# Performance work log

Measured on AMD Instinct MI355X. Metric: run time of the kernel, lower is better.

Reference implementation:

```python
import jax, jax.numpy as jnp
import numpy as np

D_MODEL = 512
D_QK = 512
H = 8
HEAD_DIM = D_QK // H   # 64
V_DIM = D_MODEL // H   # 64
PROJ_OUT = D_MODEL + 2 * D_QK + H  # 1544


def setup_inputs() -> dict:
    key = jax.random.key(0)
    k1, k2, k3, k4, k5 = jax.random.split(key, 5)
    B, S = 2, 2048
    x = jax.random.normal(k1, (B, S, D_MODEL), dtype=jnp.float32)
    s_in = 1.0 / np.sqrt(D_MODEL)
    Wvqkn_w = jax.random.uniform(k2, (PROJ_OUT, D_MODEL), jnp.float32, -s_in, s_in)
    Wvqkn_b = jax.random.uniform(k3, (PROJ_OUT,), jnp.float32, -s_in, s_in)
    out_w = jax.random.uniform(k4, (D_MODEL, D_MODEL), jnp.float32, -s_in, s_in)
    out_b = jax.random.uniform(k5, (D_MODEL,), jnp.float32, -s_in, s_in)
    return {"x": x, "Wvqkn_w": Wvqkn_w, "Wvqkn_b": Wvqkn_b,
            "out_w": out_w, "out_b": out_b}


def reference(x, Wvqkn_w, Wvqkn_b, out_w, out_b):
    B, S, _ = x.shape
    # fused qkvn projection
    vqkn = jnp.einsum('bsd,od->bso', x, Wvqkn_w) + Wvqkn_b  # [B,S,1544]
    v = vqkn[..., :D_MODEL]                                  # [B,S,512]
    qk = vqkn[..., D_MODEL:D_MODEL + 2 * D_QK]               # [B,S,1024]
    n = vqkn[..., D_MODEL + 2 * D_QK:]                       # [B,S,H]
    qk = qk.reshape(B, S, 2, H, HEAD_DIM)
    v = v.reshape(B, S, H, V_DIM)
    q, k = qk[:, :, 0], qk[:, :, 1]                          # approx_fn = identity
    # linear attention via cumulative KV state (scale=1.0, scale_B=False)
    kv = jnp.einsum('bshd,bsht->bshdt', k, v)                # [B,S,H,D,Dv]
    kv = jnp.cumsum(kv, axis=1)
    out = jnp.einsum('bshd,bshdt->bsht', q, kv)              # [B,S,H,Dv]
    # normalization gating: norm_fn = exp, no offset
    gate = jnp.exp(-jnp.exp(n))                              # [B,S,H]
    ctx = gate[..., None] * out
    ctx = ctx.reshape(B, S, D_MODEL)
    return jnp.einsum('bsd,od->bso', ctx, out_w) + out_b
```

## Files before the change

### kernel.cpp

```cpp
#include <hip/hip_runtime.h>
#include <hip/hip_bf16.h>
#include <math.h>

#define B_    2
#define S_    2048
#define DM    512
#define H_    8
#define PROJ  1544
#define NPAD1 1664
#define CHK   64
#define NC    32
#define BS_   4096
#define BH    16

typedef __attribute__((ext_vector_type(8))) short shortx8;
typedef __attribute__((ext_vector_type(4))) short shortx4;
typedef __attribute__((ext_vector_type(4))) float floatx4;

#define GCAST(p) ((const __attribute__((address_space(1))) void*)(p))
#define LCAST(p) ((__attribute__((address_space(3))) void*)(p))

__device__ inline short f2bf(float f) {
    __hip_bfloat16 h = __float2bfloat16(f);
    return *(short*)&h;
}
__device__ inline float bf2f(short s) {
    __hip_bfloat16 h = *(__hip_bfloat16*)&s;
    return __bfloat162float(h);
}
__device__ inline shortx8 read8(const short* buf, int row, int k) {
    return *(const shortx8*)&buf[row * 64 + ((((k >> 3) ^ (row & 7))) << 3)];
}

#define E1 ((size_t)BS_ * DM)
#define E2 ((size_t)NPAD1 * DM)
#define E3 ((size_t)DM * DM)
__global__ __launch_bounds__(256) void convert_all(const float* __restrict__ x,
                                                   const float* __restrict__ w1,
                                                   const float* __restrict__ w2,
                                                   short* __restrict__ xb,
                                                   short* __restrict__ w1b,
                                                   short* __restrict__ w2b) {
    size_t e = ((size_t)blockIdx.x * 256 + threadIdx.x) * 8;
    const float* src;
    short* dst;
    bool zero = false;
    if (e < E1) { src = x + e; dst = xb + e; }
    else if (e < E1 + E2) {
        size_t o = e - E1;
        dst = w1b + o;
        size_t row = o >> 9;
        if (row < PROJ) src = w1 + o; else { src = w1; zero = true; }
    } else if (e < E1 + E2 + E3) {
        size_t o = e - E1 - E2;
        src = w2 + o; dst = w2b + o;
    } else return;
    short out[8];
    if (zero) {
#pragma unroll
        for (int i = 0; i < 8; i++) out[i] = 0;
    } else {
        float4 f0 = *(const float4*)src;
        float4 f1 = *(const float4*)(src + 4);
        out[0] = f2bf(f0.x); out[1] = f2bf(f0.y); out[2] = f2bf(f0.z); out[3] = f2bf(f0.w);
        out[4] = f2bf(f1.x); out[5] = f2bf(f1.y); out[6] = f2bf(f1.z); out[7] = f2bf(f1.w);
    }
    *(shortx8*)dst = *(shortx8*)out;
}

__global__ __launch_bounds__(256) void gemm_mfma64(const short* __restrict__ A,
                                                   const short* __restrict__ Bw,
                                                   const float* __restrict__ bias,
                                                   float* __restrict__ C,
                                                   int N, int K) {
    __shared__ __align__(16) short As[64 * 64];
    __shared__ __align__(16) short Bs[128 * 64];
    const int tid  = threadIdx.x;
    const int wave = tid >> 6, lane = tid & 63;
    const int m0 = blockIdx.y * 64;
    const int n0 = blockIdx.x * 128;
    const int lrow = lane >> 3;
    const int swz  = ((lane & 7) ^ lrow) << 3;
    const int lm = lane & 15, q = lane >> 4;
    const int wc = wave * 32;
    floatx4 acc[4][2] = {};

    const short* gA0 = A  + (size_t)(m0 +      wave * 8 + lrow) * K + swz;
    const short* gA1 = A  + (size_t)(m0 + 32 + wave * 8 + lrow) * K + swz;
    const short* gB[4];
#pragma unroll
    for (int h = 0; h < 4; h++)
        gB[h] = Bw + (size_t)(n0 + h * 32 + wave * 8 + lrow) * K + swz;

    for (int k0 = 0; k0 < K; k0 += 64) {
        __builtin_amdgcn_global_load_lds(GCAST(gA0 + k0), LCAST(&As[(wave * 8) * 64]),        16, 0, 0);
        __builtin_amdgcn_global_load_lds(GCAST(gA1 + k0), LCAST(&As[(32 + wave * 8) * 64]),   16, 0, 0);
#pragma unroll
        for (int h = 0; h < 4; h++)
            __builtin_amdgcn_global_load_lds(GCAST(gB[h] + k0), LCAST(&Bs[(h * 32 + wave * 8) * 64]), 16, 0, 0);
        __syncthreads();
        shortx8 af[2][4], bw[2][2];
#pragma unroll
        for (int ks = 0; ks < 2; ks++) {
#pragma unroll
            for (int i = 0; i < 4; i++) af[ks][i] = read8(As, i * 16 + lm, ks * 32 + q * 8);
#pragma unroll
            for (int j = 0; j < 2; j++) bw[ks][j] = read8(Bs, wc + j * 16 + lm, ks * 32 + q * 8);
        }
#pragma unroll
        for (int ks = 0; ks < 2; ks++)
#pragma unroll
            for (int i = 0; i < 4; i++)
#pragma unroll
                for (int j = 0; j < 2; j++)
                    acc[i][j] = __builtin_amdgcn_mfma_f32_16x16x32_bf16(af[ks][i], bw[ks][j], acc[i][j], 0, 0, 0);
        __syncthreads();
    }
#pragma unroll
    for (int i = 0; i < 4; i++) {
        int rb = m0 + i * 16 + q * 4;
#pragma unroll
        for (int j = 0; j < 2; j++) {
            int col = n0 + wc + j * 16 + lm;
            float bv = bias[col];
#pragma unroll
            for (int r = 0; r < 4; r++)
                C[(size_t)(rb + r) * N + col] = acc[i][j][r] + bv;
        }
    }
}

__global__ __launch_bounds__(256) void gemm1_fused(const short* __restrict__ A,
                                                   const short* __restrict__ Bw,
                                                   const float* __restrict__ bias,
                                                   short* __restrict__ qb,
                                                   short* __restrict__ kb,
                                                   short* __restrict__ kTb,
                                                   short* __restrict__ vTb,
                                                   float* __restrict__ gateb) {
    __shared__ __align__(16) short As[64 * 64];
    __shared__ __align__(16) short Bs[128 * 64];
    const int K = DM;
    const int tid  = threadIdx.x;
    const int wave = tid >> 6, lane = tid & 63;
    const int m0 = blockIdx.y * 64;
    const int n0 = blockIdx.x * 128;
    const int lrow = lane >> 3;
    const int swz  = ((lane & 7) ^ lrow) << 3;
    const int lm = lane & 15, q = lane >> 4;
    const int wc = wave * 32;
    floatx4 acc[4][2] = {};

    const short* gA0 = A  + (size_t)(m0 +      wave * 8 + lrow) * K + swz;
    const short* gA1 = A  + (size_t)(m0 + 32 + wave * 8 + lrow) * K + swz;
    const short* gB[4];
#pragma unroll
    for (int h = 0; h < 4; h++)
        gB[h] = Bw + (size_t)(n0 + h * 32 + wave * 8 + lrow) * K + swz;

    for (int k0 = 0; k0 < K; k0 += 64) {
        __builtin_amdgcn_global_load_lds(GCAST(gA0 + k0), LCAST(&As[(wave * 8) * 64]),        16, 0, 0);
        __builtin_amdgcn_global_load_lds(GCAST(gA1 + k0), LCAST(&As[(32 + wave * 8) * 64]),   16, 0, 0);
#pragma unroll
        for (int h = 0; h < 4; h++)
            __builtin_amdgcn_global_load_lds(GCAST(gB[h] + k0), LCAST(&Bs[(h * 32 + wave * 8) * 64]), 16, 0, 0);
        __syncthreads();
        shortx8 af[2][4], bw[2][2];
#pragma unroll
        for (int ks = 0; ks < 2; ks++) {
#pragma unroll
            for (int i = 0; i < 4; i++) af[ks][i] = read8(As, i * 16 + lm, ks * 32 + q * 8);
#pragma unroll
            for (int j = 0; j < 2; j++) bw[ks][j] = read8(Bs, wc + j * 16 + lm, ks * 32 + q * 8);
        }
#pragma unroll
        for (int ks = 0; ks < 2; ks++)
#pragma unroll
            for (int i = 0; i < 4; i++)
#pragma unroll
                for (int j = 0; j < 2; j++)
                    acc[i][j] = __builtin_amdgcn_mfma_f32_16x16x32_bf16(af[ks][i], bw[ks][j], acc[i][j], 0, 0, 0);
        __syncthreads();
    }

    const int bIdx = m0 >> 11;
    const int bh0  = bIdx * H_;
#pragma unroll
    for (int i = 0; i < 4; i++) {
        int s0 = (m0 & (S_ - 1)) + i * 16 + q * 4;
#pragma unroll
        for (int j = 0; j < 2; j++) {
            int col = n0 + wc + j * 16 + lm;
            float bv = (col < PROJ) ? bias[col] : 0.f;
            float vals[4];
#pragma unroll
            for (int r = 0; r < 4; r++) vals[r] = acc[i][j][r] + bv;
            if (col < 512) {
                int h = col >> 6, vd = col & 63;
                short tmp[4];
#pragma unroll
                for (int r = 0; r < 4; r++) tmp[r] = f2bf(vals[r]);
                *(shortx4*)&vTb[((size_t)(bh0 + h) * 64 + vd) * S_ + s0] = *(shortx4*)tmp;
            } else if (col < 1024) {
                int h = (col >> 6) - 8, d = col & 63;
                size_t rb = ((size_t)(bh0 + h) * S_ + s0) * 64 + d;
#pragma unroll
                for (int r = 0; r < 4; r++) qb[rb + (size_t)r * 64] = f2bf(vals[r]);
            } else if (col < 1536) {
                int h = (col >> 6) - 16, d = col & 63;
                size_t rb = ((size_t)(bh0 + h) * S_ + s0) * 64 + d;
                short tmp[4];
#pragma unroll
                for (int r = 0; r < 4; r++) { tmp[r] = f2bf(vals[r]); kb[rb + (size_t)r * 64] = tmp[r]; }
                *(shortx4*)&kTb[((size_t)(bh0 + h) * 64 + d) * S_ + s0] = *(shortx4*)tmp;
            } else if (col < PROJ) {
                int h = col - 1536;
                float g[4];
#pragma unroll
                for (int r = 0; r < 4; r++) g[r] = __expf(-__expf(vals[r]));
                *(float4*)&gateb[(size_t)(bh0 + h) * S_ + s0] = make_float4(g[0], g[1], g[2], g[3]);
            }
        }
    }
}

__global__ __launch_bounds__(256) void chunk_kv_mfma(const short* __restrict__ vTb,
                                                     const short* __restrict__ kTb,
                                                     float* __restrict__ kvbuf) {
    __shared__ __align__(16) short VT[64 * 64];
    __shared__ __align__(16) short KT[64 * 64];
    const int blk = blockIdx.x;
    const int c = blk & (NC - 1), bh = blk >> 5;
    const int base = c * CHK;
    const int tid = threadIdx.x, wave = tid >> 6, lane = tid & 63;
    const int lrow = lane >> 3, lgrp = lane & 7;

#pragma unroll
    for (int half = 0; half < 2; half++) {
        int v0 = wave * 8 + half * 32;
        int row = v0 + lrow;
        int gcol = ((lgrp ^ (row & 7)) << 3);
        __builtin_amdgcn_global_load_lds(GCAST(vTb + ((size_t)(bh * 64 + row)) * S_ + base + gcol),
                                         LCAST(&VT[v0 * 64]), 16, 0, 0);
        __builtin_amdgcn_global_load_lds(GCAST(kTb + ((size_t)(bh * 64 + row)) * S_ + base + gcol),
                                         LCAST(&KT[v0 * 64]), 16, 0, 0);
    }
    __syncthreads();

    const int lm = lane & 15, q = lane >> 4;
    const int wr = (wave >> 1) * 32, wc = (wave & 1) * 32;
    floatx4 acc[2][2] = {};
#pragma unroll
    for (int ks = 0; ks < 2; ks++) {
        shortx8 a[2], b2[2];
#pragma unroll
        for (int i = 0; i < 2; i++) a[i]  = read8(VT, wr + i * 16 + lm, ks * 32 + q * 8);
#pragma unroll
        for (int j = 0; j < 2; j++) b2[j] = read8(KT, wc + j * 16 + lm, ks * 32 + q * 8);
#pragma unroll
        for (int i = 0; i < 2; i++)
#pragma unroll
            for (int j = 0; j < 2; j++)
                acc[i][j] = __builtin_amdgcn_mfma_f32_16x16x32_bf16(a[i], b2[j], acc[i][j], 0, 0, 0);
    }
    float* outp = kvbuf + ((size_t)blk << 12);
#pragma unroll
    for (int i = 0; i < 2; i++)
#pragma unroll
        for (int j = 0; j < 2; j++)
#pragma unroll
            for (int r = 0; r < 4; r++)
                outp[(wr + i * 16 + q * 4 + r) * 64 + wc + j * 16 + lm] = acc[i][j][r];
}

__global__ __launch_bounds__(256) void scan_groups(const float* __restrict__ kvbuf,
                                                   float* __restrict__ kvg) {
    const int blk = blockIdx.x;
    const int bh = blk >> 4, seg = blk & 15;
    const int e = seg * 256 + threadIdx.x;
    const float* src = kvbuf + (((size_t)bh * NC) << 12) + e;
    float* dst = kvg + (((size_t)bh * 8) << 12) + e;
    float run = 0.f;
#pragma unroll
    for (int g = 0; g < 8; g++) {
        dst[(size_t)g << 12] = run;
#pragma unroll
        for (int cc = 0; cc < 4; cc++)
            run += src[(size_t)(g * 4 + cc) << 12];
    }
}

__global__ __launch_bounds__(256) void attn_mfma(const short* __restrict__ qb,
                                                 const short* __restrict__ kb,
                                                 const short* __restrict__ vTb,
                                                 const float* __restrict__ gateb,
                                                 const float* __restrict__ kvbuf,
                                                 const float* __restrict__ kvg,
                                                 short* __restrict__ ctxb) {
    __shared__ __align__(16) short Qs[64 * 64];
    __shared__ __align__(16) short Ks[64 * 64];
    __shared__ __align__(16) short VTs[64 * 64];
    __shared__ __align__(16) short Phi[64 * 64];
    __shared__ __align__(16) short Plo[64 * 64];
    __shared__ __align__(16) short Sb[64 * 72];
    __shared__ float gs[64];
    const int blk = blockIdx.x;
    const int bh = blk & (BH - 1);
    const int c  = (NC - 1) - (blk >> 4);
    const int base = c * CHK;
    const int tid = threadIdx.x, wave = tid >> 6, lane = tid & 63;
    const int lrow = lane >> 3, lgrp = lane & 7;

#pragma unroll
    for (int half = 0; half < 2; half++) {
        int v0 = wave * 8 + half * 32;
        int row = v0 + lrow;
        int gcol = ((lgrp ^ (row & 7)) << 3);
        __builtin_amdgcn_global_load_lds(GCAST(qb + ((size_t)bh * S_ + base + row) * 64 + gcol),
                                         LCAST(&Qs[v0 * 64]), 16, 0, 0);
        __builtin_amdgcn_global_load_lds(GCAST(kb + ((size_t)bh * S_ + base + row) * 64 + gcol),
                                         LCAST(&Ks[v0 * 64]), 16, 0, 0);
        __builtin_amdgcn_global_load_lds(GCAST(vTb + ((size_t)(bh * 64 + row)) * S_ + base + gcol),
                                         LCAST(&VTs[v0 * 64]), 16, 0, 0);
    }

    float pacc[16];
    {
        const float* gp = kvg + (((size_t)bh * 8 + (c >> 2)) << 12) + tid;
#pragma unroll
        for (int it = 0; it < 16; it++) pacc[it] = gp[it * 256];
        const float* kvb = kvbuf + (((size_t)bh * NC) << 12) + tid;
        for (int cp = c & ~3; cp < c; cp++) {
            const float* p = kvb + ((size_t)cp << 12);
#pragma unroll
            for (int it = 0; it < 16; it++) pacc[it] += p[it * 256];
        }
    }
#pragma unroll
    for (int it = 0; it < 16; it++) {
        int idx = it * 256 + tid;
        int v = idx >> 6, d = idx & 63;
        float f = pacc[it];
        short hi = f2bf(f);
        short lo = f2bf(f - bf2f(hi));
        int sw = v * 64 + (((d >> 3) ^ (v & 7)) << 3) + (d & 7);
        Phi[sw] = hi; Plo[sw] = lo;
    }
    if (tid < 64) gs[tid] = gateb[(size_t)bh * S_ + base + tid];
    __syncthreads();

    const int lm = lane & 15, q = lane >> 4;
    const int wr = (wave >> 1) * 32, wc = (wave & 1) * 32;

    floatx4 sacc[2][2] = {};
#pragma unroll
    for (int ks = 0; ks < 2; ks++) {
        shortx8 qa[2], kf[2];
#pragma unroll
        for (int i = 0; i < 2; i++) qa[i] = read8(Qs, wr + i * 16 + lm, ks * 32 + q * 8);
#pragma unroll
        for (int j = 0; j < 2; j++) kf[j] = read8(Ks, wc + j * 16 + lm, ks * 32 + q * 8);
#pragma unroll
        for (int i = 0; i < 2; i++)
#pragma unroll
            for (int j = 0; j < 2; j++)
                sacc[i][j] = __builtin_amdgcn_mfma_f32_16x16x32_bf16(qa[i], kf[j], sacc[i][j], 0, 0, 0);
    }
#pragma unroll
    for (int i = 0; i < 2; i++)
#pragma unroll
        for (int j = 0; j < 2; j++)
#pragma unroll
            for (int r = 0; r < 4; r++) {
                int s = wr + i * 16 + q * 4 + r;
                int t = wc + j * 16 + lm;
                Sb[s * 72 + t] = f2bf(t <= s ? sacc[i][j][r] : 0.f);
            }
    __syncthreads();

    floatx4 oacc[2][2] = {};
#pragma unroll
    for (int ks = 0; ks < 2; ks++) {
        shortx8 sa[2], vb[2];
#pragma unroll
        for (int i = 0; i < 2; i++)
            sa[i] = *(const shortx8*)&Sb[(wr + i * 16 + lm) * 72 + ks * 32 + q * 8];
#pragma unroll
        for (int j = 0; j < 2; j++) vb[j] = read8(VTs, wc + j * 16 + lm, ks * 32 + q * 8);
#pragma unroll
        for (int i = 0; i < 2; i++)
#pragma unroll
            for (int j = 0; j < 2; j++)
                oacc[i][j] = __builtin_amdgcn_mfma_f32_16x16x32_bf16(sa[i], vb[j], oacc[i][j], 0, 0, 0);
    }
#pragma unroll
    for (int ks = 0; ks < 2; ks++) {
        shortx8 qa[2], ph[2], pl[2];
#pragma unroll
        for (int i = 0; i < 2; i++) qa[i] = read8(Qs, wr + i * 16 + lm, ks * 32 + q * 8);
#pragma unroll
        for (int j = 0; j < 2; j++) {
            ph[j] = read8(Phi, wc + j * 16 + lm, ks * 32 + q * 8);
            pl[j] = read8(Plo, wc + j * 16 + lm, ks * 32 + q * 8);
        }
#pragma unroll
        for (int i = 0; i < 2; i++)
#pragma unroll
            for (int j = 0; j < 2; j++) {
                oacc[i][j] = __builtin_amdgcn_mfma_f32_16x16x32_bf16(qa[i], ph[j], oacc[i][j], 0, 0, 0);
                oacc[i][j] = __builtin_amdgcn_mfma_f32_16x16x32_bf16(qa[i], pl[j], oacc[i][j], 0, 0, 0);
            }
    }
    const size_t tok0 = (size_t)(bh >> 3) * S_ + base;
    const int h = bh & 7;
#pragma unroll
    for (int i = 0; i < 2; i++)
#pragma unroll
        for (int j = 0; j < 2; j++)
#pragma unroll
            for (int r = 0; r < 4; r++) {
                int s = wr + i * 16 + q * 4 + r;
                int v = wc + j * 16 + lm;
                ctxb[(tok0 + s) * DM + h * 64 + v] = f2bf(gs[s] * oacc[i][j][r]);
            }
}

extern "C" void kernel_launch(void* const* d_in, const int* in_sizes, int n_in,
                              void* d_out, int out_size, void* d_ws, size_t ws_size,
                              hipStream_t stream) {
    const float* x       = (const float*)d_in[0];
    const float* Wvqkn_w = (const float*)d_in[1];
    const float* Wvqkn_b = (const float*)d_in[2];
    const float* out_w   = (const float*)d_in[3];
    const float* out_b   = (const float*)d_in[4];
    float* out = (float*)d_out;

    float* kvbuf = (float*)d_ws;
    float* kvg   = kvbuf + (size_t)BH * NC * 4096;
    short* xb    = (short*)(kvg + (size_t)BH * 8 * 4096);
    short* w1b   = xb   + (size_t)BS_ * DM;
    short* w2b   = w1b  + (size_t)NPAD1 * DM;
    short* ctxb  = w2b  + (size_t)DM * DM;
    short* qb    = ctxb + (size_t)BS_ * DM;
    short* kb    = qb   + (size_t)BH * S_ * 64;
    short* kTb   = kb   + (size_t)BH * S_ * 64;
    short* vTb   = kTb  + (size_t)BH * S_ * 64;
    float* gateb = (float*)(vTb + (size_t)BH * S_ * 64);

    convert_all<<<(int)((E1 + E2 + E3) / 8 / 256), 256, 0, stream>>>(
        x, Wvqkn_w, out_w, xb, w1b, w2b);

    gemm1_fused<<<dim3(NPAD1 / 128, BS_ / 64), 256, 0, stream>>>(
        xb, w1b, Wvqkn_b, qb, kb, kTb, vTb, gateb);

    chunk_kv_mfma<<<BH * NC, 256, 0, stream>>>(vTb, kTb, kvbuf);
    scan_groups<<<BH * 16, 256, 0, stream>>>(kvbuf, kvg);
    attn_mfma<<<BH * NC, 256, 0, stream>>>(qb, kb, vTb, gateb, kvbuf, kvg, ctxb);

    gemm_mfma64<<<dim3(DM / 128, BS_ / 64), 256, 0, stream>>>(ctxb, w2b, out_b, out, DM, DM);
}
```

Measured before the change: 109.7 us.

## Fuse chunk KV, scan and attention into one cooperative kernel; enlarge GEMM1 tile

Three middle kernels (per-chunk KV outer products, group scan, chunked attention) are merged into one cooperative kernel that uses grid-wide syncs between phases and keeps the K^T/V^T chunk tiles in LDS across phases. The scan now stores per-group sums, and each block accumulates the prefix from these at read time. Separately, the projection GEMM tile grows from 64x128 to 128x128 with a 2x2 wave layout, giving more reuse per block but fewer blocks. Costs are two grid barriers, 512 co-resident blocks, and higher LDS and register use.

```diff
diff --git a/kernel.cpp b/kernel.cpp
--- a/kernel.cpp
+++ b/kernel.cpp
@@ -1,6 +1,9 @@
 #include <hip/hip_runtime.h>
 #include <hip/hip_bf16.h>
+#include <hip/hip_cooperative_groups.h>
 #include <math.h>
+
+namespace cg = cooperative_groups;
 
 #define B_    2
 #define S_    2048
@@ -138,47 +141,48 @@
                                                    short* __restrict__ kTb,
                                                    short* __restrict__ vTb,
                                                    float* __restrict__ gateb) {
-    __shared__ __align__(16) short As[64 * 64];
+    __shared__ __align__(16) short As[128 * 64];
     __shared__ __align__(16) short Bs[128 * 64];
     const int K = DM;
     const int tid  = threadIdx.x;
     const int wave = tid >> 6, lane = tid & 63;
-    const int m0 = blockIdx.y * 64;
+    const int m0 = blockIdx.y * 128;
     const int n0 = blockIdx.x * 128;
     const int lrow = lane >> 3;
     const int swz  = ((lane & 7) ^ lrow) << 3;
     const int lm = lane & 15, q = lane >> 4;
-    const int wc = wave * 32;
-    floatx4 acc[4][2] = {};
-
-    const short* gA0 = A  + (size_t)(m0 +      wave * 8 + lrow) * K + swz;
-    const short* gA1 = A  + (size_t)(m0 + 32 + wave * 8 + lrow) * K + swz;
+    const int wr = (wave >> 1) * 64, wc = (wave & 1) * 64;
+    floatx4 acc[4][4] = {};
+
+    const short* gA[4];
     const short* gB[4];
 #pragma unroll
-    for (int h = 0; h < 4; h++)
+    for (int h = 0; h < 4; h++) {
+        gA[h] = A  + (size_t)(m0 + h * 32 + wave * 8 + lrow) * K + swz;
         gB[h] = Bw + (size_t)(n0 + h * 32 + wave * 8 + lrow) * K + swz;
+    }
 
     for (int k0 = 0; k0 < K; k0 += 64) {
-        __builtin_amdgcn_global_load_lds(GCAST(gA0 + k0), LCAST(&As[(wave * 8) * 64]),        16, 0, 0);
-        __builtin_amdgcn_global_load_lds(GCAST(gA1 + k0), LCAST(&As[(32 + wave * 8) * 64]),   16, 0, 0);
-#pragma unroll
-        for (int h = 0; h < 4; h++)
+#pragma unroll
+        for (int h = 0; h < 4; h++) {
+            __builtin_amdgcn_global_load_lds(GCAST(gA[h] + k0), LCAST(&As[(h * 32 + wave * 8) * 64]), 16, 0, 0);
             __builtin_amdgcn_global_load_lds(GCAST(gB[h] + k0), LCAST(&Bs[(h * 32 + wave * 8) * 64]), 16, 0, 0);
+        }
         __syncthreads();
-        shortx8 af[2][4], bw[2][2];
+        shortx8 af[2][4], bw[2][4];
 #pragma unroll
         for (int ks = 0; ks < 2; ks++) {
 #pragma unroll
-            for (int i = 0; i < 4; i++) af[ks][i] = read8(As, i * 16 + lm, ks * 32 + q * 8);
-#pragma unroll
-            for (int j = 0; j < 2; j++) bw[ks][j] = read8(Bs, wc + j * 16 + lm, ks * 32 + q * 8);
+            for (int i = 0; i < 4; i++) af[ks][i] = read8(As, wr + i * 16 + lm, ks * 32 + q * 8);
+#pragma unroll
+            for (int j = 0; j < 4; j++) bw[ks][j] = read8(Bs, wc + j * 16 + lm, ks * 32 + q * 8);
         }
 #pragma unroll
         for (int ks = 0; ks < 2; ks++)
 #pragma unroll
             for (int i = 0; i < 4; i++)
 #pragma unroll
-                for (int j = 0; j < 2; j++)
+                for (int j = 0; j < 4; j++)
                     acc[i][j] = __builtin_amdgcn_mfma_f32_16x16x32_bf16(af[ks][i], bw[ks][j], acc[i][j], 0, 0, 0);
         __syncthreads();
     }
@@ -187,9 +191,9 @@
     const int bh0  = bIdx * H_;
 #pragma unroll
     for (int i = 0; i < 4; i++) {
-        int s0 = (m0 & (S_ - 1)) + i * 16 + q * 4;
-#pragma unroll
-        for (int j = 0; j < 2; j++) {
+        int s0 = (m0 & (S_ - 1)) + wr + i * 16 + q * 4;
+#pragma unroll
+        for (int j = 0; j < 4; j++) {
             int col = n0 + wc + j * 16 + lm;
             float bv = (col < PROJ) ? bias[col] : 0.f;
             float vals[4];
@@ -224,158 +228,143 @@
     }
 }
 
-__global__ __launch_bounds__(256) void chunk_kv_mfma(const short* __restrict__ vTb,
-                                                     const short* __restrict__ kTb,
-                                                     float* __restrict__ kvbuf) {
-    __shared__ __align__(16) short VT[64 * 64];
-    __shared__ __align__(16) short KT[64 * 64];
-    const int blk = blockIdx.x;
-    const int c = blk & (NC - 1), bh = blk >> 5;
-    const int base = c * CHK;
-    const int tid = threadIdx.x, wave = tid >> 6, lane = tid & 63;
-    const int lrow = lane >> 3, lgrp = lane & 7;
-
-#pragma unroll
-    for (int half = 0; half < 2; half++) {
-        int v0 = wave * 8 + half * 32;
-        int row = v0 + lrow;
-        int gcol = ((lgrp ^ (row & 7)) << 3);
-        __builtin_amdgcn_global_load_lds(GCAST(vTb + ((size_t)(bh * 64 + row)) * S_ + base + gcol),
-                                         LCAST(&VT[v0 * 64]), 16, 0, 0);
-        __builtin_amdgcn_global_load_lds(GCAST(kTb + ((size_t)(bh * 64 + row)) * S_ + base + gcol),
-                                         LCAST(&KT[v0 * 64]), 16, 0, 0);
-    }
-    __syncthreads();
-
-    const int lm = lane & 15, q = lane >> 4;
-    const int wr = (wave >> 1) * 32, wc = (wave & 1) * 32;
-    floatx4 acc[2][2] = {};
-#pragma unroll
-    for (int ks = 0; ks < 2; ks++) {
-        shortx8 a[2], b2[2];
-#pragma unroll
-        for (int i = 0; i < 2; i++) a[i]  = read8(VT, wr + i * 16 + lm, ks * 32 + q * 8);
-#pragma unroll
-        for (int j = 0; j < 2; j++) b2[j] = read8(KT, wc + j * 16 + lm, ks * 32 + q * 8);
-#pragma unroll
-        for (int i = 0; i < 2; i++)
-#pragma unroll
-            for (int j = 0; j < 2; j++)
-                acc[i][j] = __builtin_amdgcn_mfma_f32_16x16x32_bf16(a[i], b2[j], acc[i][j], 0, 0, 0);
-    }
-    float* outp = kvbuf + ((size_t)blk << 12);
-#pragma unroll
-    for (int i = 0; i < 2; i++)
-#pragma unroll
-        for (int j = 0; j < 2; j++)
-#pragma unroll
-            for (int r = 0; r < 4; r++)
-                outp[(wr + i * 16 + q * 4 + r) * 64 + wc + j * 16 + lm] = acc[i][j][r];
-}
-
-__global__ __launch_bounds__(256) void scan_groups(const float* __restrict__ kvbuf,
-                                                   float* __restrict__ kvg) {
-    const int blk = blockIdx.x;
-    const int bh = blk >> 4, seg = blk & 15;
-    const int e = seg * 256 + threadIdx.x;
-    const float* src = kvbuf + (((size_t)bh * NC) << 12) + e;
-    float* dst = kvg + (((size_t)bh * 8) << 12) + e;
-    float run = 0.f;
-#pragma unroll
-    for (int g = 0; g < 8; g++) {
-        dst[(size_t)g << 12] = run;
-#pragma unroll
-        for (int cc = 0; cc < 4; cc++)
-            run += src[(size_t)(g * 4 + cc) << 12];
-    }
-}
-
-__global__ __launch_bounds__(256) void attn_mfma(const short* __restrict__ qb,
-                                                 const short* __restrict__ kb,
-                                                 const short* __restrict__ vTb,
-                                                 const float* __restrict__ gateb,
-                                                 const float* __restrict__ kvbuf,
-                                                 const float* __restrict__ kvg,
-                                                 short* __restrict__ ctxb) {
+__global__ __launch_bounds__(256) void middle_fused(const short* __restrict__ qb,
+                                                    const short* __restrict__ kb,
+                                                    const short* __restrict__ kTb,
+                                                    const short* __restrict__ vTb,
+                                                    const float* __restrict__ gateb,
+                                                    float* __restrict__ kvbuf,
+                                                    float* __restrict__ kvg,
+                                                    short* __restrict__ ctxb) {
     __shared__ __align__(16) short Qs[64 * 64];
     __shared__ __align__(16) short Ks[64 * 64];
-    __shared__ __align__(16) short VTs[64 * 64];
+    __shared__ __align__(16) short KT[64 * 64];
+    __shared__ __align__(16) short VT[64 * 64];
     __shared__ __align__(16) short Phi[64 * 64];
     __shared__ __align__(16) short Plo[64 * 64];
     __shared__ __align__(16) short Sb[64 * 72];
     __shared__ float gs[64];
+    cg::grid_group grid = cg::this_grid();
     const int blk = blockIdx.x;
-    const int bh = blk & (BH - 1);
-    const int c  = (NC - 1) - (blk >> 4);
+    const int bh = blk >> 5, c = blk & 31;
     const int base = c * CHK;
     const int tid = threadIdx.x, wave = tid >> 6, lane = tid & 63;
-    const int lrow = lane >> 3, lgrp = lane & 7;
+    const int lrow8 = lane >> 3, lgrp = lane & 7;
 
 #pragma unroll
     for (int half = 0; half < 2; half++) {
         int v0 = wave * 8 + half * 32;
-        int row = v0 + lrow;
+        int row = v0 + lrow8;
         int gcol = ((lgrp ^ (row & 7)) << 3);
         __builtin_amdgcn_global_load_lds(GCAST(qb + ((size_t)bh * S_ + base + row) * 64 + gcol),
                                          LCAST(&Qs[v0 * 64]), 16, 0, 0);
         __builtin_amdgcn_global_load_lds(GCAST(kb + ((size_t)bh * S_ + base + row) * 64 + gcol),
                                          LCAST(&Ks[v0 * 64]), 16, 0, 0);
+        __builtin_amdgcn_global_load_lds(GCAST(kTb + ((size_t)(bh * 64 + row)) * S_ + base + gcol),
+                                         LCAST(&KT[v0 * 64]), 16, 0, 0);
         __builtin_amdgcn_global_load_lds(GCAST(vTb + ((size_t)(bh * 64 + row)) * S_ + base + gcol),
-                                         LCAST(&VTs[v0 * 64]), 16, 0, 0);
-    }
-
-    float pacc[16];
-    {
-        const float* gp = kvg + (((size_t)bh * 8 + (c >> 2)) << 12) + tid;
-#pragma unroll
-        for (int it = 0; it < 16; it++) pacc[it] = gp[it * 256];
-        const float* kvb = kvbuf + (((size_t)bh * NC) << 12) + tid;
-        for (int cp = c & ~3; cp < c; cp++) {
-            const float* p = kvb + ((size_t)cp << 12);
-#pragma unroll
-            for (int it = 0; it < 16; it++) pacc[it] += p[it * 256];
-        }
-    }
-#pragma unroll
-    for (int it = 0; it < 16; it++) {
-        int idx = it * 256 + tid;
-        int v = idx >> 6, d = idx & 63;
-        float f = pacc[it];
-        short hi = f2bf(f);
-        short lo = f2bf(f - bf2f(hi));
-        int sw = v * 64 + (((d >> 3) ^ (v & 7)) << 3) + (d & 7);
-        Phi[sw] = hi; Plo[sw] = lo;
-    }
-    if (tid < 64) gs[tid] = gateb[(size_t)bh * S_ + base + tid];
+                                         LCAST(&VT[v0 * 64]), 16, 0, 0);
+    }
     __syncthreads();
 
     const int lm = lane & 15, q = lane >> 4;
     const int wr = (wave >> 1) * 32, wc = (wave & 1) * 32;
 
-    floatx4 sacc[2][2] = {};
-#pragma unroll
-    for (int ks = 0; ks < 2; ks++) {
-        shortx8 qa[2], kf[2];
-#pragma unroll
-        for (int i = 0; i < 2; i++) qa[i] = read8(Qs, wr + i * 16 + lm, ks * 32 + q * 8);
-#pragma unroll
-        for (int j = 0; j < 2; j++) kf[j] = read8(Ks, wc + j * 16 + lm, ks * 32 + q * 8);
+    {
+        floatx4 uacc[2][2] = {};
+#pragma unroll
+        for (int ks = 0; ks < 2; ks++) {
+            shortx8 a[2], b2[2];
+#pragma unroll
+            for (int i = 0; i < 2; i++) a[i]  = read8(VT, wr + i * 16 + lm, ks * 32 + q * 8);
+#pragma unroll
+            for (int j = 0; j < 2; j++) b2[j] = read8(KT, wc + j * 16 + lm, ks * 32 + q * 8);
+#pragma unroll
+            for (int i = 0; i < 2; i++)
+#pragma unroll
+                for (int j = 0; j < 2; j++)
+                    uacc[i][j] = __builtin_amdgcn_mfma_f32_16x16x32_bf16(a[i], b2[j], uacc[i][j], 0, 0, 0);
+        }
+        float* outp = kvbuf + (((size_t)bh * NC + c) << 12);
 #pragma unroll
         for (int i = 0; i < 2; i++)
 #pragma unroll
             for (int j = 0; j < 2; j++)
-                sacc[i][j] = __builtin_amdgcn_mfma_f32_16x16x32_bf16(qa[i], kf[j], sacc[i][j], 0, 0, 0);
-    }
-#pragma unroll
-    for (int i = 0; i < 2; i++)
-#pragma unroll
-        for (int j = 0; j < 2; j++)
-#pragma unroll
-            for (int r = 0; r < 4; r++) {
-                int s = wr + i * 16 + q * 4 + r;
-                int t = wc + j * 16 + lm;
-                Sb[s * 72 + t] = f2bf(t <= s ? sacc[i][j][r] : 0.f);
-            }
+#pragma unroll
+                for (int r = 0; r < 4; r++)
+                    outp[(wr + i * 16 + q * 4 + r) * 64 + wc + j * 16 + lm] = uacc[i][j][r];
+    }
+    grid.sync();
+
+    if (c < 8) {
+        const float* src = kvbuf + (((size_t)bh * NC + c * 4) << 12) + tid;
+        float sums[16] = {};
+#pragma unroll
+        for (int cc = 0; cc < 4; cc++)
+#pragma unroll
+            for (int it = 0; it < 16; it++)
+                sums[it] += src[((size_t)cc << 12) + it * 256];
+        float* dst = kvg + (((size_t)bh * 8 + c) << 12) + tid;
+#pragma unroll
+        for (int it = 0; it < 16; it++) dst[it * 256] = sums[it];
+    }
+    grid.sync();
+
+    {
+        float pacc[16] = {};
+        const int g = c >> 2;
+        const float* gpb = kvg + (((size_t)bh * 8) << 12) + tid;
+        for (int gp = 0; gp < g; gp++) {
+            const float* p = gpb + ((size_t)gp << 12);
+#pragma unroll
+            for (int it = 0; it < 16; it++) pacc[it] += p[it * 256];
+        }
+        const float* kvb = kvbuf + (((size_t)bh * NC) << 12) + tid;
+        for (int cp = g * 4; cp < c; cp++) {
+            const float* p = kvb + ((size_t)cp << 12);
+#pragma unroll
+            for (int it = 0; it < 16; it++) pacc[it] += p[it * 256];
+        }
+#pragma unroll
+        for (int it = 0; it < 16; it++) {
+            int idx = it * 256 + tid;
+            int v = idx >> 6, d = idx & 63;
+            float f = pacc[it];
+            short hi = f2bf(f);
+            short lo = f2bf(f - bf2f(hi));
+            int sw = v * 64 + (((d >> 3) ^ (v & 7)) << 3) + (d & 7);
+            Phi[sw] = hi; Plo[sw] = lo;
+        }
+        if (tid < 64) gs[tid] = gateb[(size_t)bh * S_ + base + tid];
+    }
+    __syncthreads();
+
+    {
+        floatx4 sacc[2][2] = {};
+#pragma unroll
+        for (int ks = 0; ks < 2; ks++) {
+            shortx8 qa[2], kf[2];
+#pragma unroll
+            for (int i = 0; i < 2; i++) qa[i] = read8(Qs, wr + i * 16 + lm, ks * 32 + q * 8);
+#pragma unroll
+            for (int j = 0; j < 2; j++) kf[j] = read8(Ks, wc + j * 16 + lm, ks * 32 + q * 8);
+#pragma unroll
+            for (int i = 0; i < 2; i++)
+#pragma unroll
+                for (int j = 0; j < 2; j++)
+                    sacc[i][j] = __builtin_amdgcn_mfma_f32_16x16x32_bf16(qa[i], kf[j], sacc[i][j], 0, 0, 0);
+        }
+#pragma unroll
+        for (int i = 0; i < 2; i++)
+#pragma unroll
+            for (int j = 0; j < 2; j++)
+#pragma unroll
+                for (int r = 0; r < 4; r++) {
+                    int s = wr + i * 16 + q * 4 + r;
+                    int t = wc + j * 16 + lm;
+                    Sb[s * 72 + t] = f2bf(t <= s ? sacc[i][j][r] : 0.f);
+                }
+    }
     __syncthreads();
 
     floatx4 oacc[2][2] = {};
@@ -386,7 +375,7 @@
         for (int i = 0; i < 2; i++)
             sa[i] = *(const shortx8*)&Sb[(wr + i * 16 + lm) * 72 + ks * 32 + q * 8];
 #pragma unroll
-        for (int j = 0; j < 2; j++) vb[j] = read8(VTs, wc + j * 16 + lm, ks * 32 + q * 8);
+        for (int j = 0; j < 2; j++) vb[j] = read8(VT, wc + j * 16 + lm, ks * 32 + q * 8);
 #pragma unroll
         for (int i = 0; i < 2; i++)
 #pragma unroll
@@ -450,12 +439,15 @@
     convert_all<<<(int)((E1 + E2 + E3) / 8 / 256), 256, 0, stream>>>(
         x, Wvqkn_w, out_w, xb, w1b, w2b);
 
-    gemm1_fused<<<dim3(NPAD1 / 128, BS_ / 64), 256, 0, stream>>>(
+    gemm1_fused<<<dim3(NPAD1 / 128, BS_ / 128), 256, 0, stream>>>(
         xb, w1b, Wvqkn_b, qb, kb, kTb, vTb, gateb);
 
-    chunk_kv_mfma<<<BH * NC, 256, 0, stream>>>(vTb, kTb, kvbuf);
-    scan_groups<<<BH * 16, 256, 0, stream>>>(kvbuf, kvg);
-    attn_mfma<<<BH * NC, 256, 0, stream>>>(qb, kb, vTb, gateb, kvbuf, kvg, ctxb);
+    {
+        void* kargs[] = {(void*)&qb, (void*)&kb, (void*)&kTb, (void*)&vTb,
+                         (void*)&gateb, (void*)&kvbuf, (void*)&kvg, (void*)&ctxb};
+        hipLaunchCooperativeKernel((const void*)middle_fused, dim3(BH * NC), dim3(256),
+                                   kargs, 0, stream);
+    }
 
     gemm_mfma64<<<dim3(DM / 128, BS_ / 64), 256, 0, stream>>>(ctxb, w2b, out_b, out, DM, DM);
 }
```

Measured after the change: 266.3 us. 143% more time.
